# Optimization experiments

Hardware: AMD Instinct MI355X
Metric: run time of the kernel (lower is better)

## Reference

```python
import jax, jax.numpy as jnp
import numpy as np

EPS = 1e-6
LAMBDA_INIT = 0.8
ROPE_BASE = 10000.0
NUM_HEADS = 8


def rmsnorm(x, w):
    rms = jnp.sqrt(jnp.mean(x * x, axis=-1, keepdims=True) + EPS)
    return x / rms * w


def apply_rope(x):
    # Faithful to source: positions are taken along dim -2 of x.
    # Here x has shape (B, r, H, d), so rotation angle is indexed by HEAD index
    # (this mirrors the original torch code, where apply_rope is called on
    # (B, seq, H, d) tensors and uses x.shape[-2] == H for positions).
    d = x.shape[-1]
    half = d // 2  # d is even (head_dim=64)
    pos = jnp.arange(x.shape[-2])
    dim_idx = jnp.arange(half, dtype=x.dtype)
    freqs = 1.0 / (ROPE_BASE ** (dim_idx / half))
    angles = pos[:, None].astype(jnp.float32) * freqs  # (H, half)
    cos, sin = jnp.cos(angles), jnp.sin(angles)
    x1, x2 = x[..., :half], x[..., half:2 * half]
    return jnp.concatenate([x1 * cos - x2 * sin, x1 * sin + x2 * cos], axis=-1)


def linterp(x, out_size):
    # torch F.interpolate(mode='linear', align_corners=False) along axis 1 of (B, L, C)
    in_size = x.shape[1]
    scale = in_size / out_size
    coords = jnp.clip((jnp.arange(out_size) + 0.5) * scale - 0.5, 0.0, in_size - 1)
    lo = jnp.floor(coords).astype(jnp.int32)
    hi = jnp.minimum(lo + 1, in_size - 1)
    w = (coords - lo)[None, :, None].astype(x.dtype)
    return x[:, lo] * (1 - w) + x[:, hi] * w


def setup_inputs() -> dict:
    key = jax.random.key(0)
    ks = jax.random.split(key, 12)
    B, L, C = 4, 4096, 1024
    H = NUM_HEADS
    d = C // (2 * H)  # 64
    s = 0.02
    return {
        "x": jax.random.normal(ks[0], (B, L, C), jnp.float32),
        "Wq": jax.random.normal(ks[1], (C, C), jnp.float32) * s,
        "Wk": jax.random.normal(ks[2], (C, C), jnp.float32) * s,
        "Wv": jax.random.normal(ks[3], (C, C), jnp.float32) * s,
        "Wo": jax.random.normal(ks[4], (C, C), jnp.float32) * s,
        "q_norm_w": 1.0 + jax.random.normal(ks[5], (d,), jnp.float32) * s,
        "k_norm_w": 1.0 + jax.random.normal(ks[6], (d,), jnp.float32) * s,
        "head_norm_w": 1.0 + jax.random.normal(ks[7], (2 * d,), jnp.float32) * s,
        "lambda_q1": jax.random.normal(ks[8], (d,), jnp.float32) * 0.1,
        "lambda_k1": jax.random.normal(ks[9], (d,), jnp.float32) * 0.1,
        "lambda_q2": jax.random.normal(ks[10], (d,), jnp.float32) * 0.1,
        "lambda_k2": jax.random.normal(ks[11], (d,), jnp.float32) * 0.1,
    }


def reference(x, Wq, Wk, Wv, Wo, q_norm_w, k_norm_w, head_norm_w,
              lambda_q1, lambda_k1, lambda_q2, lambda_k2):
    B, L, C = x.shape
    H = NUM_HEADS
    d = C // (2 * H)
    scale = d ** -0.5
    r = max(1, int(L ** 0.75))  # 512 for L=4096

    xd = linterp(x, r)  # (B, r, C)

    q = (xd @ Wq.T).reshape(B, r, H, 2, d)
    k = (xd @ Wk.T).reshape(B, r, H, 2, d)
    v = (xd @ Wv.T).reshape(B, r, H, 2 * d)

    q1 = apply_rope(rmsnorm(q[..., 0, :], q_norm_w))
    q2 = apply_rope(rmsnorm(q[..., 1, :], q_norm_w))
    k1 = apply_rope(rmsnorm(k[..., 0, :], k_norm_w))
    k2 = apply_rope(rmsnorm(k[..., 1, :], k_norm_w))

    # (B, H, r, d)
    q1, q2 = jnp.swapaxes(q1, 1, 2), jnp.swapaxes(q2, 1, 2)
    k1, k2 = jnp.swapaxes(k1, 1, 2), jnp.swapaxes(k2, 1, 2)
    v = jnp.swapaxes(v, 1, 2)  # (B, H, r, 2d)

    lam = (jnp.exp(jnp.sum(lambda_q1 * lambda_k1))
           - jnp.exp(jnp.sum(lambda_q2 * lambda_k2)) + LAMBDA_INIT)

    attn1 = jax.nn.softmax(jnp.einsum('bhqd,bhkd->bhqk', q1, k1) * scale, axis=-1)
    attn2 = jax.nn.softmax(jnp.einsum('bhqd,bhkd->bhqk', q2, k2) * scale, axis=-1)
    diff = jnp.einsum('bhqk,bhkd->bhqd', attn1 - lam * attn2, v)  # (B,H,r,2d)

    diff = jnp.swapaxes(diff, 1, 2)  # (B, r, H, 2d)
    diff = rmsnorm(diff, head_norm_w) * (1.0 - LAMBDA_INIT)
    lowrank_out = jax.nn.silu(diff.reshape(B, r, C) @ Wo.T)
    full_out = linterp(lowrank_out, L)
    return (full_out, lowrank_out)
```

## Files before the change

### kernel.cpp

```cpp
#include <hip/hip_runtime.h>

typedef __bf16 bf16_t;
typedef __bf16 bf16x8 __attribute__((ext_vector_type(8)));
typedef __bf16 bf16x4 __attribute__((ext_vector_type(4)));
typedef float  f32x4  __attribute__((ext_vector_type(4)));

#define MFMA16(a,b,c) __builtin_amdgcn_mfma_f32_16x16x32_bf16((a),(b),(c),0,0,0)

#define NB 4
#define LL 4096
#define CC 1024
#define HH 8
#define RR 512

__global__ void k_wcvt(const float* __restrict__ w0, const float* __restrict__ w1,
                       const float* __restrict__ w2, const float* __restrict__ w3,
                       bf16_t* __restrict__ dst) {
  const float* src = (blockIdx.y == 0) ? w0 : (blockIdx.y == 1) ? w1 : (blockIdx.y == 2) ? w2 : w3;
  int idx = blockIdx.x * 256 + threadIdx.x;
  f32x4 v = *(const f32x4*)&src[(size_t)idx * 4];
  bf16x4 o;
#pragma unroll
  for (int j = 0; j < 4; ++j) o[j] = (bf16_t)v[j];
  *(bf16x4*)&dst[(size_t)blockIdx.y * 1048576 + (size_t)idx * 4] = o;
}

__global__ void k_down(const float* __restrict__ x, bf16_t* __restrict__ xd) {
  int idx = blockIdx.x * 256 + threadIdx.x;
  int c4  = idx & 255;
  int row = idx >> 8;
  int b = row >> 9, i = row & 511;
  const float* p0 = x + (size_t)(b * LL + 8 * i + 3) * CC + c4 * 4;
  f32x4 a = *(const f32x4*)p0;
  f32x4 bb = *(const f32x4*)(p0 + CC);
  bf16x4 o;
#pragma unroll
  for (int j = 0; j < 4; ++j) o[j] = (bf16_t)(0.5f * (a[j] + bb[j]));
  *(bf16x4*)&xd[(size_t)row * CC + c4 * 4] = o;
}

template <int CH>
__device__ __forceinline__ void stage_async(const bf16_t* __restrict__ g, bf16_t* __restrict__ s, int t) {
#pragma unroll
  for (int j = 0; j < CH; ++j) {
    int c = t + j * 256;
    const bf16_t* ga = g + (c >> 2) * 1024 + (c & 3) * 8;
    bf16_t* la = s + c * 8;
    __builtin_amdgcn_global_load_lds((const __attribute__((address_space(1))) void*)ga,
                                     (__attribute__((address_space(3))) void*)la, 16, 0, 0);
  }
}

template <int MODE, int BM>
__global__ __launch_bounds__(256) void k_gemm(const bf16_t* __restrict__ A,
                                              const bf16_t* __restrict__ wbf,
                                              const float* __restrict__ qw,
                                              const float* __restrict__ kw,
                                              bf16_t* __restrict__ q1, bf16_t* __restrict__ q2,
                                              bf16_t* __restrict__ k1, bf16_t* __restrict__ k2,
                                              bf16_t* __restrict__ vt, float* __restrict__ outF) {
  __shared__ bf16_t sA[BM * 32];
  __shared__ bf16_t sB[128 * 32];
  const int z = (MODE == 0) ? blockIdx.z : 3;
  const bf16_t* W = wbf + (size_t)z * (1u << 20);
  int t = threadIdx.x;
  int lane = t & 63, w = t >> 6;
  int wr = w >> 1, wc = w & 1;
  int lr = lane & 15, quad = lane >> 4;
  int m0 = blockIdx.y * BM, n0 = blockIdx.x * 128;
  const int NI = BM / 32;
  f32x4 acc[NI][4] = {};
  for (int k0 = 0; k0 < 1024; k0 += 32) {
    __syncthreads();
    stage_async<BM / 64>(A + (size_t)m0 * 1024 + k0, sA, t);
    stage_async<2>(W + (size_t)n0 * 1024 + k0, sB, t);
    __syncthreads();
    bf16x8 af[NI], bfr[4];
#pragma unroll
    for (int i = 0; i < NI; ++i) af[i] = *(bf16x8*)&sA[(wr * (BM / 2) + i * 16 + lr) * 32 + quad * 8];
#pragma unroll
    for (int j = 0; j < 4; ++j) bfr[j] = *(bf16x8*)&sB[(wc * 64 + j * 16 + lr) * 32 + quad * 8];
#pragma unroll
    for (int i = 0; i < NI; ++i)
#pragma unroll
      for (int j = 0; j < 4; ++j)
        acc[i][j] = MFMA16(af[i], bfr[j], acc[i][j]);
  }

  if (MODE == 1) {
#pragma unroll
    for (int i = 0; i < NI; ++i)
#pragma unroll
      for (int j = 0; j < 4; ++j) {
        int row0 = m0 + wr * (BM / 2) + i * 16 + quad * 4;
        int col  = n0 + wc * 64 + j * 16 + lr;
#pragma unroll
        for (int rg = 0; rg < 4; ++rg) {
          float v = acc[i][j][rg];
          outF[(size_t)(row0 + rg) * 1024 + col] = v / (1.f + __expf(-v));
        }
      }
    return;
  }

  if (z == 2) {
#pragma unroll
    for (int i = 0; i < NI; ++i)
#pragma unroll
      for (int j = 0; j < 4; ++j) {
        int row0 = m0 + wr * (BM / 2) + i * 16 + quad * 4;
        int col  = n0 + wc * 64 + j * 16 + lr;
        int b = row0 >> 9, ii = row0 & 511;
        int h = col >> 7, nn = col & 127;
        bf16x4 pk;
#pragma unroll
        for (int rg = 0; rg < 4; ++rg) pk[rg] = (bf16_t)acc[i][j][rg];
        *(bf16x4*)&vt[(size_t)((b * HH + h) * 128 + nn) * 512 + ii] = pk;
      }
    return;
  }

  {
    const float* nw = z ? kw : qw;
    int colbase = n0 + wc * 64;
    int h = colbase >> 7;
    int slot = (colbase >> 6) & 1;
    bf16_t* dst = (z == 0) ? (slot ? q2 : q1) : (slot ? k2 : k1);
    float qs = (z == 0) ? 0.125f : 1.0f;
    float w0 = nw[lr], w1 = nw[16 + lr], w2 = nw[32 + lr], w3 = nw[48 + lr];
    const float nlog = -13.287712379549449f / 32.f;
    float f0 = exp2f((float)lr * nlog);
    float f1 = exp2f((float)(16 + lr) * nlog);
    float sn0, cs0, sn1, cs1;
    __sincosf((float)h * f0, &sn0, &cs0);
    __sincosf((float)h * f1, &sn1, &cs1);
#pragma unroll
    for (int i = 0; i < NI; ++i) {
#pragma unroll
      for (int rg = 0; rg < 4; ++rg) {
        float v0 = acc[i][0][rg], v1 = acc[i][1][rg], v2 = acc[i][2][rg], v3 = acc[i][3][rg];
        float ss = v0 * v0 + v1 * v1 + v2 * v2 + v3 * v3;
#pragma unroll
        for (int m = 1; m <= 8; m <<= 1) ss += __shfl_xor(ss, m);
        float rinv = qs / sqrtf(ss * (1.f / 64.f) + 1e-6f);
        float n0v = v0 * rinv * w0, n1v = v1 * rinv * w1, n2v = v2 * rinv * w2, n3v = v3 * rinv * w3;
        float o0 = n0v * cs0 - n2v * sn0;
        float o1 = n1v * cs1 - n3v * sn1;
        float o2 = n0v * sn0 + n2v * cs0;
        float o3 = n1v * sn1 + n3v * cs1;
        int row = m0 + wr * (BM / 2) + i * 16 + quad * 4 + rg;
        int b = row >> 9, seq = row & 511;
        size_t base = ((size_t)((b * HH + h) * RR + seq)) * 64;
        dst[base + lr]      = (bf16_t)o0;
        dst[base + 16 + lr] = (bf16_t)o1;
        dst[base + 32 + lr] = (bf16_t)o2;
        dst[base + 48 + lr] = (bf16_t)o3;
      }
    }
  }
}

__global__ __launch_bounds__(256) void k_attn(const bf16_t* __restrict__ q1, const bf16_t* __restrict__ q2,
                                              const bf16_t* __restrict__ k1, const bf16_t* __restrict__ k2,
                                              const bf16_t* __restrict__ vt,
                                              const float* __restrict__ lq1, const float* __restrict__ lk1,
                                              const float* __restrict__ lq2, const float* __restrict__ lk2,
                                              const float* __restrict__ hw, bf16_t* __restrict__ anorm) {
  __shared__ bf16_t P[16 * 520];
  __shared__ float Sm1[4][16], Sl1[4][16], Sm2[4][16], Sl2[4][16], Sq[4][16];
  int t = threadIdx.x;
  int lane = t & 63, w = t >> 6;
  int lr = lane & 15, quad = lane >> 4;
  int qt = blockIdx.x, bh = blockIdx.y;
  int b = bh >> 3, h = bh & 7;

  float t1 = lq1[lane] * lk1[lane];
  float t2 = lq2[lane] * lk2[lane];
#pragma unroll
  for (int m = 1; m <= 32; m <<= 1) { t1 += __shfl_xor(t1, m); t2 += __shfl_xor(t2, m); }
  float lam = expf(t1) - expf(t2) + 0.8f;

  const bf16_t* q1b = q1 + (size_t)(bh * RR + qt * 16) * 64;
  const bf16_t* q2b = q2 + (size_t)(bh * RR + qt * 16) * 64;
  const bf16_t* k1b = k1 + (size_t)bh * RR * 64;
  const bf16_t* k2b = k2 + (size_t)bh * RR * 64;
  const bf16_t* vtb = vt + (size_t)bh * 128 * 512;

  bf16x8 a1[2], a2[2];
#pragma unroll
  for (int kk = 0; kk < 2; ++kk) {
    a1[kk] = *(const bf16x8*)&q1b[lr * 64 + kk * 32 + quad * 8];
    a2[kk] = *(const bf16x8*)&q2b[lr * 64 + kk * 32 + quad * 8];
  }

  f32x4 s1[8], s2[8];
#pragma unroll
  for (int kt = 0; kt < 8; ++kt) {
    const bf16_t* kr = k1b + (size_t)((w * 8 + kt) * 16 + lr) * 64 + quad * 8;
    f32x4 a = {};
    a = MFMA16(a1[0], *(const bf16x8*)kr, a);
    a = MFMA16(a1[1], *(const bf16x8*)(kr + 32), a);
    s1[kt] = a;
  }
#pragma unroll
  for (int kt = 0; kt < 8; ++kt) {
    const bf16_t* kr = k2b + (size_t)((w * 8 + kt) * 16 + lr) * 64 + quad * 8;
    f32x4 a = {};
    a = MFMA16(a2[0], *(const bf16x8*)kr, a);
    a = MFMA16(a2[1], *(const bf16x8*)(kr + 32), a);
    s2[kt] = a;
  }
  float m1[4] = {-3e38f, -3e38f, -3e38f, -3e38f}, m2[4] = {-3e38f, -3e38f, -3e38f, -3e38f};
#pragma unroll
  for (int kt = 0; kt < 8; ++kt)
#pragma unroll
    for (int rg = 0; rg < 4; ++rg) { m1[rg] = fmaxf(m1[rg], s1[kt][rg]); m2[rg] = fmaxf(m2[rg], s2[kt][rg]); }
#pragma unroll
  for (int m = 1; m <= 8; m <<= 1)
#pragma unroll
    for (int rg = 0; rg < 4; ++rg) { m1[rg] = fmaxf(m1[rg], __shfl_xor(m1[rg], m)); m2[rg] = fmaxf(m2[rg], __shfl_xor(m2[rg], m)); }
  float l1[4] = {}, l2[4] = {};
#pragma unroll
  for (int kt = 0; kt < 8; ++kt)
#pragma unroll
    for (int rg = 0; rg < 4; ++rg) {
      float e1 = __expf(s1[kt][rg] - m1[rg]); s1[kt][rg] = e1; l1[rg] += e1;
      float e2 = __expf(s2[kt][rg] - m2[rg]); s2[kt][rg] = e2; l2[rg] += e2;
    }
#pragma unroll
  for (int m = 1; m <= 8; m <<= 1)
#pragma unroll
    for (int rg = 0; rg < 4; ++rg) { l1[rg] += __shfl_xor(l1[rg], m); l2[rg] += __shfl_xor(l2[rg], m); }
  if (lr == 0) {
#pragma unroll
    for (int rg = 0; rg < 4; ++rg) {
      int r = quad * 4 + rg;
      Sm1[w][r] = m1[rg]; Sl1[w][r] = l1[rg];
      Sm2[w][r] = m2[rg]; Sl2[w][r] = l2[rg];
    }
  }
  __syncthreads();
  float sc1[4], sc2[4];
#pragma unroll
  for (int rg = 0; rg < 4; ++rg) {
    int r = quad * 4 + rg;
    float gm1 = fmaxf(fmaxf(Sm1[0][r], Sm1[1][r]), fmaxf(Sm1[2][r], Sm1[3][r]));
    float L1 = Sl1[0][r] * __expf(Sm1[0][r] - gm1) + Sl1[1][r] * __expf(Sm1[1][r] - gm1)
             + Sl1[2][r] * __expf(Sm1[2][r] - gm1) + Sl1[3][r] * __expf(Sm1[3][r] - gm1);
    sc1[rg] = __expf(m1[rg] - gm1) / L1;
    float gm2 = fmaxf(fmaxf(Sm2[0][r], Sm2[1][r]), fmaxf(Sm2[2][r], Sm2[3][r]));
    float L2 = Sl2[0][r] * __expf(Sm2[0][r] - gm2) + Sl2[1][r] * __expf(Sm2[1][r] - gm2)
             + Sl2[2][r] * __expf(Sm2[2][r] - gm2) + Sl2[3][r] * __expf(Sm2[3][r] - gm2);
    sc2[rg] = lam * __expf(m2[rg] - gm2) / L2;
  }
#pragma unroll
  for (int kt = 0; kt < 8; ++kt)
#pragma unroll
    for (int rg = 0; rg < 4; ++rg) {
      float v = s1[kt][rg] * sc1[rg] - s2[kt][rg] * sc2[rg];
      P[(quad * 4 + rg) * 520 + (w * 8 + kt) * 16 + lr] = (bf16_t)v;
    }
  __syncthreads();
  f32x4 accO[2] = {};
#pragma unroll
  for (int ks = 0; ks < 16; ++ks) {
    bf16x8 pf = *(bf16x8*)&P[lr * 520 + ks * 32 + quad * 8];
#pragma unroll
    for (int j = 0; j < 2; ++j) {
      int nt = w * 2 + j;
      bf16x8 vf = *(const bf16x8*)&vtb[(size_t)(nt * 16 + lr) * 512 + ks * 32 + quad * 8];
      accO[j] = MFMA16(pf, vf, accO[j]);
    }
  }
  float ssr[4] = {};
#pragma unroll
  for (int j = 0; j < 2; ++j)
#pragma unroll
    for (int rg = 0; rg < 4; ++rg) ssr[rg] += accO[j][rg] * accO[j][rg];
#pragma unroll
  for (int m = 1; m <= 8; m <<= 1)
#pragma unroll
    for (int rg = 0; rg < 4; ++rg) ssr[rg] += __shfl_xor(ssr[rg], m);
  if (lr == 0) {
#pragma unroll
    for (int rg = 0; rg < 4; ++rg) Sq[w][quad * 4 + rg] = ssr[rg];
  }
  __syncthreads();
#pragma unroll
  for (int j = 0; j < 2; ++j) {
    int nt = w * 2 + j;
    float wcol = hw[nt * 16 + lr];
#pragma unroll
    for (int rg = 0; rg < 4; ++rg) {
      int r = quad * 4 + rg;
      float tot = Sq[0][r] + Sq[1][r] + Sq[2][r] + Sq[3][r];
      float rinv = 0.2f / sqrtf(tot * (1.f / 128.f) + 1e-6f);
      int i = qt * 16 + r;
      anorm[(size_t)(b * RR + i) * 1024 + h * 128 + nt * 16 + lr] = (bf16_t)(accO[j][rg] * rinv * wcol);
    }
  }
}

__global__ void k_up(const float* __restrict__ lrk, float* __restrict__ out) {
  int j = blockIdx.x;
  int b = blockIdx.y;
  int c = threadIdx.x * 4;
  float coord = 0.125f * (float)j - 0.4375f;
  coord = fminf(fmaxf(coord, 0.f), 511.f);
  int lo = (int)floorf(coord);
  int hi = lo + 1 < 511 ? lo + 1 : 511;
  float w = coord - (float)lo;
  f32x4 a = *(const f32x4*)&lrk[(size_t)(b * RR + lo) * CC + c];
  f32x4 bb = *(const f32x4*)&lrk[(size_t)(b * RR + hi) * CC + c];
  f32x4 o;
#pragma unroll
  for (int t = 0; t < 4; ++t) o[t] = a[t] * (1.f - w) + bb[t] * w;
  *(f32x4*)&out[(size_t)(b * LL + j) * CC + c] = o;
}

extern "C" void kernel_launch(void* const* d_in, const int* in_sizes, int n_in,
                              void* d_out, int out_size, void* d_ws, size_t ws_size,
                              hipStream_t stream) {
  (void)in_sizes; (void)n_in; (void)out_size; (void)ws_size;
  const float* x   = (const float*)d_in[0];
  const float* Wq  = (const float*)d_in[1];
  const float* Wk  = (const float*)d_in[2];
  const float* Wv  = (const float*)d_in[3];
  const float* Wo  = (const float*)d_in[4];
  const float* qw  = (const float*)d_in[5];
  const float* kw  = (const float*)d_in[6];
  const float* hw  = (const float*)d_in[7];
  const float* lq1 = (const float*)d_in[8];
  const float* lk1 = (const float*)d_in[9];
  const float* lq2 = (const float*)d_in[10];
  const float* lk2 = (const float*)d_in[11];
  float* out = (float*)d_out;

  char* ws = (char*)d_ws;
  bf16_t* wbf   = (bf16_t*)(ws);
  bf16_t* xd    = (bf16_t*)(ws + (8u << 20));
  bf16_t* vt    = (bf16_t*)(ws + (12u << 20));
  bf16_t* q1    = (bf16_t*)(ws + (16u << 20));
  bf16_t* q2    = (bf16_t*)(ws + (18u << 20));
  bf16_t* k1    = (bf16_t*)(ws + (20u << 20));
  bf16_t* k2    = (bf16_t*)(ws + (22u << 20));
  bf16_t* anorm = (bf16_t*)(ws + (24u << 20));

  float* lowrank = out + (size_t)NB * LL * CC;

  k_wcvt<<<dim3(1024, 4), 256, 0, stream>>>(Wq, Wk, Wv, Wo, wbf);
  k_down<<<2048, 256, 0, stream>>>(x, xd);
  k_gemm<0, 128><<<dim3(8, 16, 3), 256, 0, stream>>>(xd, wbf, qw, kw, q1, q2, k1, k2, vt, nullptr);
  k_attn<<<dim3(32, 32), 256, 0, stream>>>(q1, q2, k1, k2, vt, lq1, lk1, lq2, lk2, hw, anorm);
  k_gemm<1, 64><<<dim3(8, 32, 1), 256, 0, stream>>>(anorm, wbf, qw, kw, nullptr, nullptr, nullptr, nullptr, nullptr, lowrank);
  k_up<<<dim3(4096, 4), 256, 0, stream>>>(lowrank, out);
}
```

Baseline: 239.1 us.

## Triple-buffer GEMM LDS staging with async prefetch and merge prep kernels

The GEMM main loop moves from a single LDS buffer with two barriers per k-step to a three-stage ring buffer. Global-to-LDS loads for step k+2 are issued while step k computes, and manual vmcnt waits replace the second barrier. The weight-conversion and downsample kernels are also merged into one launch to save a kernel launch. The cost is triple the LDS footprint, which may reduce occupancy, and the hand-written waitcnt counts must match the number of loads issued per stage.

Result: no change. 237.4 us (-0.7%).

```diff
diff --git a/kernel.cpp b/kernel.cpp
--- a/kernel.cpp
+++ b/kernel.cpp
@@ -13,30 +13,33 @@
 #define HH 8
 #define RR 512
 
-__global__ void k_wcvt(const float* __restrict__ w0, const float* __restrict__ w1,
+__global__ void k_prep(const float* __restrict__ x,
+                       const float* __restrict__ w0, const float* __restrict__ w1,
                        const float* __restrict__ w2, const float* __restrict__ w3,
-                       bf16_t* __restrict__ dst) {
-  const float* src = (blockIdx.y == 0) ? w0 : (blockIdx.y == 1) ? w1 : (blockIdx.y == 2) ? w2 : w3;
-  int idx = blockIdx.x * 256 + threadIdx.x;
-  f32x4 v = *(const f32x4*)&src[(size_t)idx * 4];
-  bf16x4 o;
-#pragma unroll
-  for (int j = 0; j < 4; ++j) o[j] = (bf16_t)v[j];
-  *(bf16x4*)&dst[(size_t)blockIdx.y * 1048576 + (size_t)idx * 4] = o;
-}
-
-__global__ void k_down(const float* __restrict__ x, bf16_t* __restrict__ xd) {
-  int idx = blockIdx.x * 256 + threadIdx.x;
-  int c4  = idx & 255;
-  int row = idx >> 8;
-  int b = row >> 9, i = row & 511;
-  const float* p0 = x + (size_t)(b * LL + 8 * i + 3) * CC + c4 * 4;
-  f32x4 a = *(const f32x4*)p0;
-  f32x4 bb = *(const f32x4*)(p0 + CC);
-  bf16x4 o;
-#pragma unroll
-  for (int j = 0; j < 4; ++j) o[j] = (bf16_t)(0.5f * (a[j] + bb[j]));
-  *(bf16x4*)&xd[(size_t)row * CC + c4 * 4] = o;
+                       bf16_t* __restrict__ wbf, bf16_t* __restrict__ xd) {
+  int bid = blockIdx.x;
+  if (bid < 4096) {
+    int y = bid >> 10;
+    const float* src = (y == 0) ? w0 : (y == 1) ? w1 : (y == 2) ? w2 : w3;
+    int idx = (bid & 1023) * 256 + threadIdx.x;
+    f32x4 v = *(const f32x4*)&src[(size_t)idx * 4];
+    bf16x4 o;
+#pragma unroll
+    for (int j = 0; j < 4; ++j) o[j] = (bf16_t)v[j];
+    *(bf16x4*)&wbf[(size_t)y * 1048576 + (size_t)idx * 4] = o;
+  } else {
+    int idx = (bid - 4096) * 256 + threadIdx.x;
+    int c4  = idx & 255;
+    int row = idx >> 8;
+    int b = row >> 9, i = row & 511;
+    const float* p0 = x + (size_t)(b * LL + 8 * i + 3) * CC + c4 * 4;
+    f32x4 a = *(const f32x4*)p0;
+    f32x4 bb = *(const f32x4*)(p0 + CC);
+    bf16x4 o;
+#pragma unroll
+    for (int j = 0; j < 4; ++j) o[j] = (bf16_t)(0.5f * (a[j] + bb[j]));
+    *(bf16x4*)&xd[(size_t)row * CC + c4 * 4] = o;
+  }
 }
 
 template <int CH>
@@ -59,8 +62,8 @@
                                               bf16_t* __restrict__ q1, bf16_t* __restrict__ q2,
                                               bf16_t* __restrict__ k1, bf16_t* __restrict__ k2,
                                               bf16_t* __restrict__ vt, float* __restrict__ outF) {
-  __shared__ bf16_t sA[BM * 32];
-  __shared__ bf16_t sB[128 * 32];
+  __shared__ bf16_t sA[3][BM * 32];
+  __shared__ bf16_t sB[3][128 * 32];
   const int z = (MODE == 0) ? blockIdx.z : 3;
   const bf16_t* W = wbf + (size_t)z * (1u << 20);
   int t = threadIdx.x;
@@ -68,23 +71,45 @@
   int wr = w >> 1, wc = w & 1;
   int lr = lane & 15, quad = lane >> 4;
   int m0 = blockIdx.y * BM, n0 = blockIdx.x * 128;
-  const int NI = BM / 32;
+  constexpr int NI = BM / 32;
   f32x4 acc[NI][4] = {};
-  for (int k0 = 0; k0 < 1024; k0 += 32) {
-    __syncthreads();
-    stage_async<BM / 64>(A + (size_t)m0 * 1024 + k0, sA, t);
-    stage_async<2>(W + (size_t)n0 * 1024 + k0, sB, t);
-    __syncthreads();
+
+  const bf16_t* Ab = A + (size_t)m0 * 1024;
+  const bf16_t* Wb = W + (size_t)n0 * 1024;
+
+  stage_async<BM / 64>(Ab, sA[0], t);
+  stage_async<2>(Wb, sB[0], t);
+  stage_async<BM / 64>(Ab + 32, sA[1], t);
+  stage_async<2>(Wb + 32, sB[1], t);
+
+  int cur = 0, stg = 2;
+#pragma unroll 1
+  for (int it = 0; it < 32; ++it) {
+    if (it < 31) {
+      if constexpr (BM == 128) asm volatile("s_waitcnt vmcnt(4) lgkmcnt(0)" ::: "memory");
+      else                     asm volatile("s_waitcnt vmcnt(3) lgkmcnt(0)" ::: "memory");
+    } else {
+      asm volatile("s_waitcnt vmcnt(0) lgkmcnt(0)" ::: "memory");
+    }
+    __builtin_amdgcn_s_barrier();
+    if (it < 30) {
+      stage_async<BM / 64>(Ab + (it + 2) * 32, sA[stg], t);
+      stage_async<2>(Wb + (it + 2) * 32, sB[stg], t);
+    }
+    const bf16_t* cA = sA[cur];
+    const bf16_t* cB = sB[cur];
     bf16x8 af[NI], bfr[4];
 #pragma unroll
-    for (int i = 0; i < NI; ++i) af[i] = *(bf16x8*)&sA[(wr * (BM / 2) + i * 16 + lr) * 32 + quad * 8];
-#pragma unroll
-    for (int j = 0; j < 4; ++j) bfr[j] = *(bf16x8*)&sB[(wc * 64 + j * 16 + lr) * 32 + quad * 8];
+    for (int i = 0; i < NI; ++i) af[i] = *(const bf16x8*)&cA[(wr * (BM / 2) + i * 16 + lr) * 32 + quad * 8];
+#pragma unroll
+    for (int j = 0; j < 4; ++j) bfr[j] = *(const bf16x8*)&cB[(wc * 64 + j * 16 + lr) * 32 + quad * 8];
 #pragma unroll
     for (int i = 0; i < NI; ++i)
 #pragma unroll
       for (int j = 0; j < 4; ++j)
         acc[i][j] = MFMA16(af[i], bfr[j], acc[i][j]);
+    cur = (cur == 2) ? 0 : cur + 1;
+    stg = (stg == 2) ? 0 : stg + 1;
   }
 
   if (MODE == 1) {
@@ -348,8 +373,7 @@
 
   float* lowrank = out + (size_t)NB * LL * CC;
 
-  k_wcvt<<<dim3(1024, 4), 256, 0, stream>>>(Wq, Wk, Wv, Wo, wbf);
-  k_down<<<2048, 256, 0, stream>>>(x, xd);
+  k_prep<<<6144, 256, 0, stream>>>(x, Wq, Wk, Wv, Wo, wbf, xd);
   k_gemm<0, 128><<<dim3(8, 16, 3), 256, 0, stream>>>(xd, wbf, qw, kw, q1, q2, k1, k2, vt, nullptr);
   k_attn<<<dim3(32, 32), 256, 0, stream>>>(q1, q2, k1, k2, vt, lq1, lk1, lq2, lk2, hw, anorm);
   k_gemm<1, 64><<<dim3(8, 32, 1), 256, 0, stream>>>(anorm, wbf, qw, kw, nullptr, nullptr, nullptr, nullptr, nullptr, lowrank);
```
